# Kernel tuning notes

Hardware: AMD Instinct MI355X
Metric: run time of the kernel (lower is better)

## Reference

```python
import jax, jax.numpy as jnp
import numpy as np

B, N, E = 4, 8192, 131072
NODE_F, EDGE_F, HID, ACT = 16, 1, 128, 8


def _glorot(key, shape):
    fan_in, fan_out = shape[0], shape[1]
    lim = np.sqrt(6.0 / (fan_in + fan_out))
    return jax.random.uniform(key, shape, jnp.float32, -lim, lim)


def setup_inputs() -> dict:
    key = jax.random.key(0)
    ks = jax.random.split(key, 20)
    inp = {
        'node_features': jax.random.randint(ks[0], (B, N, NODE_F), 0, 10, jnp.int32),
        'edge_index': jax.random.randint(ks[1], (B, 2, E), 0, N, jnp.int64),
        'edge_features': jax.random.normal(ks[2], (B, E, EDGE_F), jnp.float32),
        # conv1: in = 2*NODE_F + EDGE_F
        'c1_w1': _glorot(ks[3], (2 * NODE_F + EDGE_F, HID)), 'c1_b1': jnp.zeros((HID,), jnp.float32),
        'c1_w2': _glorot(ks[4], (HID, HID)), 'c1_b2': jnp.zeros((HID,), jnp.float32),
        # conv2/conv3: in = 2*HID + 1
        'c2_w1': _glorot(ks[5], (2 * HID + 1, HID)), 'c2_b1': jnp.zeros((HID,), jnp.float32),
        'c2_w2': _glorot(ks[6], (HID, HID)), 'c2_b2': jnp.zeros((HID,), jnp.float32),
        'c3_w1': _glorot(ks[7], (2 * HID + 1, HID)), 'c3_b1': jnp.zeros((HID,), jnp.float32),
        'c3_w2': _glorot(ks[8], (HID, HID)), 'c3_b2': jnp.zeros((HID,), jnp.float32),
        'lin_w': _glorot(ks[9], (NODE_F + HID, ACT)), 'lin_b': jnp.zeros((ACT,), jnp.float32),
    }
    return inp


def _edge_conv(x, src, dst, ea, w1, b1, w2, b2):
    # message: cat([x_i (target), x_j (source), edge_attr]) -> Linear -> LeakyReLU -> Linear
    m = jnp.concatenate([x[dst], x[src], ea], axis=1)          # [E, 2F+EF]
    m = jax.nn.leaky_relu(m @ w1 + b1) @ w2 + b2               # [E, out]
    out = jax.ops.segment_min(m, dst, num_segments=x.shape[0])  # min-aggregate at targets
    cnt = jnp.zeros((x.shape[0],), m.dtype).at[dst].add(1.0)
    return jnp.where(cnt[:, None] > 0, out, 0.0)                # nodes w/o in-edges -> 0 (PyG)


def _graph_fwd(x0, ei, ea, p):
    x0 = x0.astype(jnp.float32)  # torch casts to IntTensor then MLP promotes; math on integer values
    src, dst = ei[0], ei[1]      # flow='source_to_target'
    x = jax.nn.leaky_relu(_edge_conv(x0, src, dst, ea, p['c1_w1'], p['c1_b1'], p['c1_w2'], p['c1_b2']))
    x = jax.nn.leaky_relu(_edge_conv(x, src, dst, ea, p['c2_w1'], p['c2_b1'], p['c2_w2'], p['c2_b2']))
    x = jax.nn.leaky_relu(_edge_conv(x, src, dst, ea, p['c3_w1'], p['c3_b1'], p['c3_w2'], p['c3_b2']))
    x = jnp.concatenate([x0, x], axis=1)
    return jax.nn.softplus(x @ p['lin_w'] + p['lin_b'])         # [N, ACT]


def reference(node_features, edge_index, edge_features,
              c1_w1, c1_b1, c1_w2, c1_b2,
              c2_w1, c2_b1, c2_w2, c2_b2,
              c3_w1, c3_b1, c3_w2, c3_b2,
              lin_w, lin_b):
    p = dict(c1_w1=c1_w1, c1_b1=c1_b1, c1_w2=c1_w2, c1_b2=c1_b2,
             c2_w1=c2_w1, c2_b1=c2_b1, c2_w2=c2_w2, c2_b2=c2_b2,
             c3_w1=c3_w1, c3_b1=c3_b1, c3_w2=c3_w2, c3_b2=c3_b2,
             lin_w=lin_w, lin_b=lin_b)
    return jax.vmap(lambda x, ei, ea: _graph_fwd(x, ei, ea, p))(
        node_features, edge_index, edge_features)               # [B, N, ACT]
```

## Files before the change

### kernel.cpp

```cpp
#include <hip/hip_runtime.h>

#define B_ 4
#define N_ 8192
#define E_ 131072
#define HID_ 128

typedef unsigned short us8 __attribute__((ext_vector_type(8)));
typedef unsigned short us4 __attribute__((ext_vector_type(4)));
typedef unsigned int   ui4 __attribute__((ext_vector_type(4)));
typedef int            i4  __attribute__((ext_vector_type(4)));
typedef __bf16         v8bf __attribute__((ext_vector_type(8)));
typedef _Float16       hf8 __attribute__((ext_vector_type(8)));
typedef float          v4f  __attribute__((ext_vector_type(4)));
typedef float          v2f  __attribute__((ext_vector_type(2)));

#define KEY_INF 0xFF800000u

__device__ __forceinline__ float b2f(unsigned short u) {
    return __uint_as_float(((unsigned)u) << 16);
}
__device__ __forceinline__ unsigned short f2b(float f) {
    unsigned x = __float_as_uint(f);
    return (unsigned short)((x + 0x7fffu + ((x >> 16) & 1u)) >> 16);
}
__device__ __forceinline__ unsigned short f2h(float f) {
    union { _Float16 h; unsigned short u; } c; c.h = (_Float16)f; return c.u;
}
__device__ __forceinline__ unsigned fkey(float f) {
    unsigned b = __float_as_uint(f);
    return (b & 0x80000000u) ? ~b : (b | 0x80000000u);
}
__device__ __forceinline__ float funkey(unsigned k) {
    unsigned b = (k & 0x80000000u) ? (k ^ 0x80000000u) : ~k;
    return __uint_as_float(b);
}

__device__ __forceinline__ void repack_one(const float* __restrict__ w1, const float* __restrict__ w2,
                                           unsigned short* __restrict__ w1n, unsigned short* __restrict__ w2t,
                                           int F, int KPAD, int gid) {
    int t1 = 256 * KPAD;
    if (gid < t1) {
        int j = gid / KPAD, k = gid - j * KPAD;
        float v = 0.f;
        if (k < F) v = (j < 128) ? w1[k * 128 + j] : w1[(F + k) * 128 + (j - 128)];
        w1n[gid] = f2b(v);
    } else {
        int g = gid - t1;
        if (g < 16384) { int j = g >> 7, k = g & 127; w2t[g] = f2h(w2[k * 128 + j]); }
    }
}

__global__ void k_setup(const int* __restrict__ nf, unsigned short* __restrict__ x0b,
                        unsigned* __restrict__ cnt, unsigned* __restrict__ agg,
                        const float* __restrict__ w1a, const float* __restrict__ w2a,
                        const float* __restrict__ w1b, const float* __restrict__ w2b,
                        const float* __restrict__ w1c, const float* __restrict__ w2c,
                        unsigned short* __restrict__ w1n0, unsigned short* __restrict__ w2t0,
                        unsigned short* __restrict__ w1n1, unsigned short* __restrict__ w2t1,
                        unsigned short* __restrict__ w1n2, unsigned short* __restrict__ w2t2) {
    const int bid = blockIdx.x, tid = threadIdx.x;
    if (bid >= 4096) {
        const int rb = bid - 4096;
        const int gid = rb * 256 + tid;
        if (rb < 96)       repack_one(w1a, w2a, w1n0, w2t0, 16, 32, gid);
        else if (rb < 288) repack_one(w1b, w2b, w1n1, w2t1, 128, 128, gid - 96 * 256);
        else               repack_one(w1c, w2c, w1n2, w2t2, 128, 128, gid - 288 * 256);
        return;
    }
    const int gid = bid * 256 + tid;
    ui4 v = {KEY_INF, KEY_INF, KEY_INF, KEY_INF};
    ((ui4*)agg)[gid] = v;
    if (bid < 512) {
        i4 x = ((const i4*)nf)[gid];
        us4 o;
        o[0] = f2b((float)x[0]); o[1] = f2b((float)x[1]);
        o[2] = f2b((float)x[2]); o[3] = f2b((float)x[3]);
        ((us4*)x0b)[gid] = o;
    }
    if (bid < 128) cnt[gid] = 0u;
}

__global__ void k_hist(const int* __restrict__ ei, unsigned* __restrict__ cnt) {
    int gid = blockIdx.x * 256 + threadIdx.x;
    int b = gid >> 17, e = gid & (E_ - 1);
    int dst = ei[(b << 18) + E_ + e];
    atomicAdd(&cnt[(b << 13) + dst], 1u);
}

__global__ __launch_bounds__(1024) void k_scan(unsigned* __restrict__ cnt) {
    int b = blockIdx.x;
    __shared__ unsigned ps[1024];
    unsigned* c = cnt + (b << 13) + threadIdx.x * 8;
    unsigned loc[8]; unsigned s = 0;
#pragma unroll
    for (int i = 0; i < 8; i++) { loc[i] = c[i]; s += loc[i]; }
    ps[threadIdx.x] = s;
    __syncthreads();
    for (int off = 1; off < 1024; off <<= 1) {
        unsigned v = (threadIdx.x >= (unsigned)off) ? ps[threadIdx.x - off] : 0u;
        __syncthreads();
        ps[threadIdx.x] += v;
        __syncthreads();
    }
    unsigned run = ps[threadIdx.x] - s;
#pragma unroll
    for (int i = 0; i < 8; i++) { c[i] = run; run += loc[i]; }
}

template<int KPAD, bool FROM_AGG>
__device__ __forceinline__ void node_body(
    int bid,
    const unsigned short* __restrict__ xin,
    unsigned* __restrict__ agg,
    const unsigned short* __restrict__ w1n,
    const float* __restrict__ bias1,
    unsigned short* __restrict__ Yd,
    unsigned short* __restrict__ Ys,
    char* smem)
{
    constexpr int ASTR = KPAD + 8;
    unsigned short* A  = (unsigned short*)smem;
    unsigned short* Yb = (unsigned short*)(smem + 64 * ASTR * 2);

    const int tid = threadIdx.x;
    const int wave = tid >> 6, lane = tid & 63, lq = lane >> 4, lm = lane & 15;
    const int tile = (bid & 7) * 64 + (bid >> 3);
    const int n0 = tile * 64;

    v8bf wf[4][KPAD / 32]; float b1v[4];
#pragma unroll
    for (int nt = 0; nt < 4; nt++) {
        const int col = wave * 64 + nt * 16 + lm;
#pragma unroll
        for (int ks = 0; ks < KPAD / 32; ks++)
            wf[nt][ks] = *(const v8bf*)&w1n[col * KPAD + ks * 32 + lq * 8];
        b1v[nt] = (col < 128) ? bias1[col] : 0.f;
    }

    {
        const int row = tid >> 2, p = tid & 3;
        if (FROM_AGG) {
#pragma unroll
            for (int i = 0; i < 8; i++) {
                const int c = p + 4 * i;
                unsigned* ap = agg + ((size_t)(n0 + row)) * 128 + c * 4;
                ui4 k = *(ui4*)ap;
                ui4 inf = {KEY_INF, KEY_INF, KEY_INF, KEY_INF};
                *(ui4*)ap = inf;
                us4 o;
#pragma unroll
                for (int j = 0; j < 4; j++) {
                    float v = (k[j] == KEY_INF) ? 0.f : funkey(k[j]);
                    v = (v > 0.f) ? v : 0.01f * v;
                    o[j] = f2b(v);
                }
                *(us4*)&A[row * ASTR + c * 4] = o;
            }
        } else {
            us4 v = *(const us4*)(xin + ((size_t)(n0 + row)) * 16 + p * 4);
            *(us4*)&A[row * ASTR + p * 4] = v;
            us4 z = {0, 0, 0, 0};
            *(us4*)&A[row * ASTR + 16 + p * 4] = z;
        }
    }
    __syncthreads();

#pragma unroll
    for (int mt = 0; mt < 4; mt++) {
        v4f acc[4];
#pragma unroll
        for (int nt = 0; nt < 4; nt++) acc[nt] = v4f{0.f, 0.f, 0.f, 0.f};
#pragma unroll
        for (int ks = 0; ks < KPAD / 32; ks++) {
            v8bf a = *(const v8bf*)&A[(mt * 16 + lm) * ASTR + ks * 32 + lq * 8];
#pragma unroll
            for (int nt = 0; nt < 4; nt++)
                acc[nt] = __builtin_amdgcn_mfma_f32_16x16x32_bf16(a, wf[nt][ks], acc[nt], 0, 0, 0);
        }
#pragma unroll
        for (int nt = 0; nt < 4; nt++) {
            const int col = wave * 64 + nt * 16 + lm;
#pragma unroll
            for (int r = 0; r < 4; r++)
                Yb[(mt * 16 + lq * 4 + r) * 264 + col] = f2h(acc[nt][r] + b1v[nt]);
        }
    }
    __syncthreads();

    const int bb = tile >> 7, nl0 = (tile & 127) * 64;
#pragma unroll
    for (int i = 0; i < 8; i++) {
        const int idx = tid + 256 * i;
        const int row = idx >> 5, c = idx & 31;
        us8 v = *(const us8*)&Yb[row * 264 + c * 8];
        const int col0 = c * 8;
        unsigned short* dp = (col0 < 128)
            ? (Yd + ((size_t)(bb * N_) + nl0 + row) * 128 + col0)
            : (Ys + ((size_t)(bb * N_) + nl0 + row) * 128 + (col0 - 128));
        *(us8*)dp = v;
    }
}

template<int KPAD>
__global__ __launch_bounds__(256, 3) void k_node(
    const unsigned short* __restrict__ xin, unsigned* __restrict__ agg,
    const unsigned short* __restrict__ w1n, const float* __restrict__ bias1,
    unsigned short* __restrict__ Yd, unsigned short* __restrict__ Ys)
{
    __shared__ __align__(16) char smem[64 * (KPAD + 8) * 2 + 64 * 264 * 2];
    node_body<KPAD, true>(blockIdx.x, xin, agg, w1n, bias1, Yd, Ys, smem);
}

__global__ __launch_bounds__(256, 3) void k_scat_node1(
    const int* __restrict__ ei, unsigned* __restrict__ wptr, int* __restrict__ perm,
    const unsigned short* __restrict__ x0b,
    const unsigned short* __restrict__ w1n, const float* __restrict__ bias1,
    unsigned short* __restrict__ Yd, unsigned short* __restrict__ Ys)
{
    __shared__ __align__(16) char smem[64 * 40 * 2 + 64 * 264 * 2];
    const int bid = blockIdx.x;
    if (bid < 2048) {
        int gid = bid * 256 + threadIdx.x;
        int b = gid >> 17, e = gid & (E_ - 1);
        int dst = ei[(b << 18) + E_ + e];
        unsigned pos = atomicAdd(&wptr[(b << 13) + dst], 1u);
        perm[(b << 17) + pos] = e;
        return;
    }
    node_body<32, false>(bid - 2048, x0b, (unsigned*)nullptr, w1n, bias1, Yd, Ys, smem);
}

__global__ __launch_bounds__(256, 4) void k_edge(
    const unsigned short* __restrict__ Yd,
    const unsigned short* __restrict__ Ys,
    const int* __restrict__ ei,
    const float* __restrict__ eaf,
    const int* __restrict__ perm,
    const unsigned short* __restrict__ w2t,
    const float* __restrict__ weap,
    const float* __restrict__ bias2,
    unsigned* __restrict__ agg)
{
    __shared__ __align__(16) unsigned short Hs[2][64 * 128];
    __shared__ __align__(16) int      dstl[2][64];
    __shared__ __align__(16) _Float16 weal[128];

    const int tid = threadIdx.x;
    const int wave = tid >> 6, lane = tid & 63, lq = lane >> 4, lm = lane & 15;

    if (tid < 128) weal[tid] = (_Float16)weap[tid];

    hf8 w2f[2][4]; float b2v[2];
#pragma unroll
    for (int nt = 0; nt < 2; nt++) {
        const int col = wave * 32 + nt * 16 + lm;
#pragma unroll
        for (int ks = 0; ks < 4; ks++)
            w2f[nt][ks] = *(const hf8*)&w2t[col * 128 + ks * 32 + lq * 8];
        b2v[nt] = bias2[col];
    }
    __syncthreads();

    const int arow = tid >> 2, p = tid & 3;
    const int s = ((arow & 0x0C) << 2) | ((arow >> 2) & 0x0C) | (arow & 3);
    const int rsw = arow & 15;

    const hf8 c01v = {(_Float16)0.01f, (_Float16)0.01f, (_Float16)0.01f, (_Float16)0.01f,
                      (_Float16)0.01f, (_Float16)0.01f, (_Float16)0.01f, (_Float16)0.01f};

    int t = (blockIdx.x & 7) * 1024 + (blockIdx.x >> 3);
    int b = t >> 11;
    int e = perm[(b << 17) + (t & 2047) * 64 + s];
    int src = ei[(b << 18) + e];
    int dst = ei[(b << 18) + E_ + e];
    float ea = eaf[(b << 17) + e];

    {
        const hf8* ydp = (const hf8*)(Yd + ((size_t)(b * N_) + dst) * 128);
        const hf8* ysp = (const hf8*)(Ys + ((size_t)(b * N_) + src) * 128);
        if (p == 0) dstl[0][s] = dst;
        const _Float16 eh = (_Float16)ea;
        const hf8 ea8 = {eh, eh, eh, eh, eh, eh, eh, eh};
        hf8 va = ydp[p], vb = ysp[p];
#pragma unroll
        for (int i = 0; i < 4; i++) {
            hf8 na, nb;
            if (i < 3) { na = ydp[p + 4 * (i + 1)]; nb = ysp[p + 4 * (i + 1)]; }
            const int c = p + 4 * i;
            hf8 wv = *(const hf8*)&weal[c * 8];
            hf8 z = va + vb + wv * ea8;
            z = __builtin_elementwise_max(z, z * c01v);
            *(hf8*)&Hs[0][arow * 128 + ((c ^ rsw) * 8)] = z;
            va = na; vb = nb;
        }
    }
    __syncthreads();

    for (int jj = 0; jj < 8; jj++) {
        const int curb = b, buf = jj & 1;

        t += 128;
        if (jj < 7) {
            b = t >> 11;
            e = perm[(b << 17) + (t & 2047) * 64 + s];
            src = ei[(b << 18) + e];
            dst = ei[(b << 18) + E_ + e];
            ea = eaf[(b << 17) + e];
        }

        {
            const int col0 = wave * 32 + lm, col1 = col0 + 16;
            unsigned* aggb = agg + (size_t)(curb * N_) * 128;
            float cur0 = 0.f, cur1 = 0.f; int curd = -1;
#pragma unroll
            for (int mt = 0; mt < 4; mt++) {
                const int row = mt * 16 + lm;
                v4f acc0 = {b2v[0], b2v[0], b2v[0], b2v[0]};
                v4f acc1 = {b2v[1], b2v[1], b2v[1], b2v[1]};
#pragma unroll
                for (int ks = 0; ks < 4; ks++) {
                    hf8 a = *(const hf8*)&Hs[buf][row * 128 + (((ks * 4 + lq) ^ lm) * 8)];
                    acc0 = __builtin_amdgcn_mfma_f32_16x16x32_f16(a, w2f[0][ks], acc0, 0, 0, 0);
                    acc1 = __builtin_amdgcn_mfma_f32_16x16x32_f16(a, w2f[1][ks], acc1, 0, 0, 0);
                }
                i4 dv = *(const i4*)&dstl[buf][lq * 16 + mt * 4];
#pragma unroll
                for (int r = 0; r < 4; r++) {
                    const float v0 = acc0[r];
                    const float v1 = acc1[r];
                    const int d = dv[r];
                    if (d != curd) {
                        if (curd >= 0) {
                            atomicMin(aggb + (size_t)curd * 128 + col0, fkey(cur0));
                            atomicMin(aggb + (size_t)curd * 128 + col1, fkey(cur1));
                        }
                        curd = d; cur0 = v0; cur1 = v1;
                    } else {
                        cur0 = fminf(cur0, v0); cur1 = fminf(cur1, v1);
                    }
                }
            }
            atomicMin(aggb + (size_t)curd * 128 + col0, fkey(cur0));
            atomicMin(aggb + (size_t)curd * 128 + col1, fkey(cur1));
        }

        if (jj < 7) {
            const hf8* ydp = (const hf8*)(Yd + ((size_t)(b * N_) + dst) * 128);
            const hf8* ysp = (const hf8*)(Ys + ((size_t)(b * N_) + src) * 128);
            if (p == 0) dstl[buf ^ 1][s] = dst;
            const _Float16 eh = (_Float16)ea;
            const hf8 ea8 = {eh, eh, eh, eh, eh, eh, eh, eh};
            hf8 va = ydp[p], vb = ysp[p];
#pragma unroll
            for (int i = 0; i < 4; i++) {
                hf8 na, nb;
                if (i < 3) { na = ydp[p + 4 * (i + 1)]; nb = ysp[p + 4 * (i + 1)]; }
                const int c = p + 4 * i;
                hf8 wv = *(const hf8*)&weal[c * 8];
                hf8 z = va + vb + wv * ea8;
                z = __builtin_elementwise_max(z, z * c01v);
                *(hf8*)&Hs[buf ^ 1][arow * 128 + ((c ^ rsw) * 8)] = z;
                va = na; vb = nb;
            }
        }
        __syncthreads();
    }
}

__global__ __launch_bounds__(256, 4) void k_final(
    const unsigned short* __restrict__ x0b, const unsigned* __restrict__ agg,
    const float* __restrict__ lw, const float* __restrict__ lb,
    float* __restrict__ out) {
    __shared__ float w[144 * 8];
    __shared__ float bias8[8];
    __shared__ float xs[64 * 129];
    const int tid = threadIdx.x;
    for (int i = tid; i < 1152; i += 256) w[i] = lw[i];
    if (tid < 8) bias8[tid] = lb[tid];
    const int n0 = blockIdx.x * 64;
#pragma unroll
    for (int i = 0; i < 8; i++) {
        const int idx = tid + 256 * i;
        const int row = idx >> 5, c = idx & 31;
        ui4 k = ((const ui4*)(agg + ((size_t)(n0 + row)) * 128))[c];
#pragma unroll
        for (int j = 0; j < 4; j++) {
            float v = (k[j] == KEY_INF) ? 0.f : funkey(k[j]);
            v = fmaxf(v, 0.01f * v);
            xs[row * 129 + c * 4 + j] = v;
        }
    }
    __syncthreads();
    const int node = tid >> 2, ap = (tid & 3) * 2;
    float a0 = bias8[ap], a1 = bias8[ap + 1];
    const unsigned short* x0 = x0b + (size_t)(n0 + node) * 16;
#pragma unroll
    for (int f = 0; f < 16; f++) {
        const float xv = b2f(x0[f]);
        a0 += xv * w[f * 8 + ap]; a1 += xv * w[f * 8 + ap + 1];
    }
    const float* xr = &xs[node * 129];
#pragma unroll 8
    for (int f = 0; f < 128; f++) {
        const float xv = xr[f];
        a0 += xv * w[(16 + f) * 8 + ap]; a1 += xv * w[(16 + f) * 8 + ap + 1];
    }
    v2f o;
    o[0] = fmaxf(a0, 0.f) + log1pf(expf(-fabsf(a0)));
    o[1] = fmaxf(a1, 0.f) + log1pf(expf(-fabsf(a1)));
    *(v2f*)&out[(size_t)(n0 + node) * 8 + ap] = o;
}

extern "C" void kernel_launch(void* const* d_in, const int* in_sizes, int n_in,
                              void* d_out, int out_size, void* d_ws, size_t ws_size,
                              hipStream_t stream) {
    (void)in_sizes; (void)n_in; (void)out_size; (void)ws_size;
    const int* nf  = (const int*)d_in[0];
    const int* ei  = (const int*)d_in[1];
    const float* eaf = (const float*)d_in[2];
    const float* cw1[3] = {(const float*)d_in[3],  (const float*)d_in[7],  (const float*)d_in[11]};
    const float* cb1[3] = {(const float*)d_in[4],  (const float*)d_in[8],  (const float*)d_in[12]};
    const float* cw2[3] = {(const float*)d_in[5],  (const float*)d_in[9],  (const float*)d_in[13]};
    const float* cb2[3] = {(const float*)d_in[6],  (const float*)d_in[10], (const float*)d_in[14]};
    const float* lw = (const float*)d_in[15];
    const float* lb = (const float*)d_in[16];
    float* out = (float*)d_out;

    size_t off = 0;
    auto carve = [&](size_t bytes) { void* p = (char*)d_ws + off; off += (bytes + 255) & ~(size_t)255; return p; };
    unsigned short* x0b  = (unsigned short*)carve((size_t)B_ * N_ * 16 * 2);
    unsigned*       agg  = (unsigned*)carve((size_t)B_ * N_ * 128 * 4);
    unsigned*       cnt  = (unsigned*)carve((size_t)B_ * N_ * 4);
    int*            perm = (int*)carve((size_t)B_ * E_ * 4);
    unsigned short* Yd   = (unsigned short*)carve((size_t)B_ * N_ * 128 * 2);
    unsigned short* Ys   = (unsigned short*)carve((size_t)B_ * N_ * 128 * 2);
    unsigned short* w1n0 = (unsigned short*)carve(256 * 32 * 2);
    unsigned short* w2t0 = (unsigned short*)carve(128 * 128 * 2);
    unsigned short* w1n1 = (unsigned short*)carve(256 * 128 * 2);
    unsigned short* w2t1 = (unsigned short*)carve(128 * 128 * 2);
    unsigned short* w1n2 = (unsigned short*)carve(256 * 128 * 2);
    unsigned short* w2t2 = (unsigned short*)carve(128 * 128 * 2);

    k_setup<<<4576, 256, 0, stream>>>(nf, x0b, cnt, agg,
                                      cw1[0], cw2[0], cw1[1], cw2[1], cw1[2], cw2[2],
                                      w1n0, w2t0, w1n1, w2t1, w1n2, w2t2);
    k_hist<<<2048, 256, 0, stream>>>(ei, cnt);
    k_scan<<<B_, 1024, 0, stream>>>(cnt);

    k_scat_node1<<<2560, 256, 0, stream>>>(ei, cnt, perm, x0b, w1n0, cb1[0], Yd, Ys);
    k_edge<<<1024, 256, 0, stream>>>(Yd, Ys, ei, eaf, perm, w2t0, cw1[0] + 32 * 128, cb2[0], agg);

    k_node<128><<<512, 256, 0, stream>>>(x0b, agg, w1n1, cb1[1], Yd, Ys);
    k_edge<<<1024, 256, 0, stream>>>(Yd, Ys, ei, eaf, perm, w2t1, cw1[1] + 256 * 128, cb2[1], agg);

    k_node<128><<<512, 256, 0, stream>>>(x0b, agg, w1n2, cb1[2], Yd, Ys);
    k_edge<<<1024, 256, 0, stream>>>(Yd, Ys, ei, eaf, perm, w2t2, cw1[2] + 256 * 128, cb2[2], agg);

    k_final<<<512, 256, 0, stream>>>(x0b, agg, lw, lb, out);
}
```

Baseline: 296.6 us.

## Give each lane a contiguous sorted edge run and store interior segments without atomics

Edge-to-block assignment changes so each block handles a contiguous chunk of 512 dst-sorted edges, and each lane's 16-row quadrant walks a contiguous 128-edge stripe across the 8 iterations. The running min state now persists across iterations. Only the first and last segments of each run use atomicMin, and interior segments, which this lane alone owns, are written with plain stores. This cuts atomic traffic on the aggregation buffer. It relies on the permutation being sorted by destination, and correctness depends on interior segments being fully owned by a single lane.

```diff
diff --git a/kernel.cpp b/kernel.cpp
--- a/kernel.cpp
+++ b/kernel.cpp
@@ -261,16 +261,20 @@
     }
     __syncthreads();
 
+    const int chunk = (blockIdx.x & 7) * 128 + (blockIdx.x >> 3);
+    const int b = chunk >> 8;
+    const int ebase = (b << 17) + (chunk & 255) * 512;
+
     const int arow = tid >> 2, p = tid & 3;
-    const int s = ((arow & 0x0C) << 2) | ((arow >> 2) & 0x0C) | (arow & 3);
+    const int lqg = (arow >> 2) & 3, mtg = arow >> 4, rg = arow & 3;
+    const int sl  = lqg * 16 + mtg * 4 + rg;
+    const int se0 = lqg * 128 + mtg * 4 + rg;
     const int rsw = arow & 15;
 
     const hf8 c01v = {(_Float16)0.01f, (_Float16)0.01f, (_Float16)0.01f, (_Float16)0.01f,
                       (_Float16)0.01f, (_Float16)0.01f, (_Float16)0.01f, (_Float16)0.01f};
 
-    int t = (blockIdx.x & 7) * 1024 + (blockIdx.x >> 3);
-    int b = t >> 11;
-    int e = perm[(b << 17) + (t & 2047) * 64 + s];
+    int e   = perm[ebase + se0];
     int src = ei[(b << 18) + e];
     int dst = ei[(b << 18) + E_ + e];
     float ea = eaf[(b << 17) + e];
@@ -278,7 +282,7 @@
     {
         const hf8* ydp = (const hf8*)(Yd + ((size_t)(b * N_) + dst) * 128);
         const hf8* ysp = (const hf8*)(Ys + ((size_t)(b * N_) + src) * 128);
-        if (p == 0) dstl[0][s] = dst;
+        if (p == 0) dstl[0][sl] = dst;
         const _Float16 eh = (_Float16)ea;
         const hf8 ea8 = {eh, eh, eh, eh, eh, eh, eh, eh};
         hf8 va = ydp[p], vb = ysp[p];
@@ -296,22 +300,21 @@
     }
     __syncthreads();
 
+    const int col0 = wave * 32 + lm, col1 = col0 + 16;
+    unsigned* aggb = agg + (size_t)(b * N_) * 128;
+    float cur0 = 0.f, cur1 = 0.f; int curd = -1; bool fseg = true;
+
     for (int jj = 0; jj < 8; jj++) {
-        const int curb = b, buf = jj & 1;
-
-        t += 128;
+        const int buf = jj & 1;
+
         if (jj < 7) {
-            b = t >> 11;
-            e = perm[(b << 17) + (t & 2047) * 64 + s];
+            e   = perm[ebase + se0 + (jj + 1) * 16];
             src = ei[(b << 18) + e];
             dst = ei[(b << 18) + E_ + e];
-            ea = eaf[(b << 17) + e];
+            ea  = eaf[(b << 17) + e];
         }
 
         {
-            const int col0 = wave * 32 + lm, col1 = col0 + 16;
-            unsigned* aggb = agg + (size_t)(curb * N_) * 128;
-            float cur0 = 0.f, cur1 = 0.f; int curd = -1;
 #pragma unroll
             for (int mt = 0; mt < 4; mt++) {
                 const int row = mt * 16 + lm;
@@ -331,8 +334,16 @@
                     const int d = dv[r];
                     if (d != curd) {
                         if (curd >= 0) {
-                            atomicMin(aggb + (size_t)curd * 128 + col0, fkey(cur0));
-                            atomicMin(aggb + (size_t)curd * 128 + col1, fkey(cur1));
+                            unsigned* p0 = aggb + (size_t)curd * 128 + col0;
+                            unsigned* p1 = aggb + (size_t)curd * 128 + col1;
+                            if (fseg) {
+                                atomicMin(p0, fkey(cur0));
+                                atomicMin(p1, fkey(cur1));
+                            } else {
+                                *p0 = fkey(cur0);
+                                *p1 = fkey(cur1);
+                            }
+                            fseg = false;
                         }
                         curd = d; cur0 = v0; cur1 = v1;
                     } else {
@@ -340,14 +351,12 @@
                     }
                 }
             }
-            atomicMin(aggb + (size_t)curd * 128 + col0, fkey(cur0));
-            atomicMin(aggb + (size_t)curd * 128 + col1, fkey(cur1));
         }
 
         if (jj < 7) {
             const hf8* ydp = (const hf8*)(Yd + ((size_t)(b * N_) + dst) * 128);
             const hf8* ysp = (const hf8*)(Ys + ((size_t)(b * N_) + src) * 128);
-            if (p == 0) dstl[buf ^ 1][s] = dst;
+            if (p == 0) dstl[buf ^ 1][sl] = dst;
             const _Float16 eh = (_Float16)ea;
             const hf8 ea8 = {eh, eh, eh, eh, eh, eh, eh, eh};
             hf8 va = ydp[p], vb = ysp[p];
@@ -365,6 +374,9 @@
         }
         __syncthreads();
     }
+
+    atomicMin(aggb + (size_t)curd * 128 + col0, fkey(cur0));
+    atomicMin(aggb + (size_t)curd * 128 + col1, fkey(cur1));
 }
 
 __global__ __launch_bounds__(256, 4) void k_final(
```

After: 290.5 us. 1.02x faster.
